# Kernel optimization log

Measured on AMD Instinct MI355X. Metric: run time of the kernel, lower is better.

## Reference

```python
import math
import jax, jax.numpy as jnp
import numpy as np

B, S, D, H = 1, 4096, 1024, 16
HD = D // H


def setup_inputs() -> dict:
    key = jax.random.key(0)
    ks = jax.random.split(key, 11)
    s = 0.02
    inp = {
        "q": jax.random.normal(ks[0], (B, S, D), jnp.float32),
        "k": jax.random.normal(ks[1], (B, S, D), jnp.float32),
        "v": jax.random.normal(ks[2], (B, S, D), jnp.float32),
        # causal boolean mask, broadcastable over [B, H, S, S]
        "mask": jnp.tril(jnp.ones((S, S), jnp.bool_))[None, None],
        "Wq": jax.random.normal(ks[3], (D, D), jnp.float32) * s,
        "bq": jnp.zeros((D,), jnp.float32),
        "Wk": jax.random.normal(ks[4], (D, D), jnp.float32) * s,
        "bk": jnp.zeros((D,), jnp.float32),
        "Wv": jax.random.normal(ks[5], (D, D), jnp.float32) * s,
        "bv": jnp.zeros((D,), jnp.float32),
        "Wo": jax.random.normal(ks[6], (D, D), jnp.float32) * s,
        "bo": jnp.zeros((D,), jnp.float32),
    }
    return inp


def reference(q, k, v, mask, Wq, bq, Wk, bk, Wv, bv, Wo, bo):
    # projections (torch Linear: x @ W.T + b; here W is stored already transposed)
    qp = (q @ Wq + bq).reshape(B, S, H, HD)
    kp = (k @ Wk + bk).reshape(B, S, H, HD)
    vp = (v @ Wv + bv).reshape(B, S, H, HD)
    # scores: [B, H, S, S]
    scores = jnp.einsum("bqhd,bkhd->bhqk", qp, kp) / math.sqrt(HD)
    scores = jnp.where(mask, scores, -jnp.inf)
    attn = jax.nn.softmax(scores, axis=-1)
    # context: [B, H, S, HD] -> [B, S, D]
    ctx = jnp.einsum("bhqk,bkhd->bqhd", attn, vp).reshape(B, S, D)
    return ctx @ Wo + bo
```

## Files before the change

### kernel.cpp

```cpp
#include <hip/hip_runtime.h>
#include <hip/hip_bf16.h>


#define S_LEN 4096
#define D_DIM 1024
#define NHEAD 16
#define HDIM  64

typedef __hip_bfloat16 bf16;
typedef __attribute__((ext_vector_type(8))) short bf16x8v;
typedef __attribute__((ext_vector_type(4))) short bf16x4v;
typedef __attribute__((ext_vector_type(4))) float f32x4;

#define MFMA16(a, b, c) __builtin_amdgcn_mfma_f32_16x16x32_bf16((a), (b), (c), 0, 0, 0)
#define LOG2E 1.44269504088896340736f

__device__ __forceinline__ void async_cp16(const void* g, void* l) {
    __builtin_amdgcn_global_load_lds(
        (const __attribute__((address_space(1))) unsigned int*)g,
        (__attribute__((address_space(3))) unsigned int*)l, 16, 0, 0);
}

__device__ __forceinline__ short bf_bits(float x) {
    union { bf16 h; short s; } u; u.h = __float2bfloat16(x); return u.s;
}

__global__ __launch_bounds__(256) void cvt_bf16_k(
    const float* __restrict__ x0, const float* __restrict__ x1,
    const float* __restrict__ x2,
    bf16* __restrict__ y0, bf16* __restrict__ y1, bf16* __restrict__ y2)
{
    const float* x = (blockIdx.z == 0) ? x0 : (blockIdx.z == 1) ? x1 : x2;
    bf16*       y = (blockIdx.z == 0) ? y0 : (blockIdx.z == 1) ? y1 : y2;
    const size_t i = ((size_t)blockIdx.x * 256 + threadIdx.x);
    const float4 v = ((const float4*)x)[i];
    union { bf16 h[4]; short4 s; } u;
    u.h[0] = __float2bfloat16(v.x);
    u.h[1] = __float2bfloat16(v.y);
    u.h[2] = __float2bfloat16(v.z);
    u.h[3] = __float2bfloat16(v.w);
    ((short4*)y)[i] = u.s;
}

__global__ __launch_bounds__(256) void transpose_cvt_k(
    const float* __restrict__ W0, const float* __restrict__ W1,
    const float* __restrict__ W2, const float* __restrict__ W3,
    bf16* __restrict__ T0, bf16* __restrict__ T1,
    bf16* __restrict__ T2, bf16* __restrict__ T3)
{
    const float* W = (blockIdx.z == 0) ? W0 : (blockIdx.z == 1) ? W1
                   : (blockIdx.z == 2) ? W2 : W3;
    bf16*       Wt = (blockIdx.z == 0) ? T0 : (blockIdx.z == 1) ? T1
                   : (blockIdx.z == 2) ? T2 : T3;
    __shared__ float t[32][33];
    const int bx = blockIdx.x << 5, by = blockIdx.y << 5;
    const int tx = threadIdx.x & 31, ty = threadIdx.x >> 5;
#pragma unroll
    for (int i = 0; i < 32; i += 8)
        t[ty + i][tx] = W[(size_t)(by + ty + i) * D_DIM + bx + tx];
    __syncthreads();
#pragma unroll
    for (int i = 0; i < 32; i += 8)
        Wt[(size_t)(bx + ty + i) * D_DIM + by + tx] = __float2bfloat16(t[tx][ty + i]);
}

struct GemmJob {
    const bf16* A; const bf16* Wt; const float* bias; void* out;
    int mode; float scale;
};

__global__ __launch_bounds__(256) void gemm_k(GemmJob j0, GemmJob j1, GemmJob j2)
{
    const GemmJob j = (blockIdx.z == 0) ? j0 : (blockIdx.z == 1) ? j1 : j2;
    const int K = D_DIM;
    const int bn = blockIdx.x << 7;
    const int bm = blockIdx.y << 7;
    const int tid = threadIdx.x;
    const int w = tid >> 6, lane = tid & 63;
    const int col = lane & 15, g = lane >> 4;
    const int wr = (w >> 1) << 6, wc = (w & 1) << 6;

    __shared__ bf16 As[128 * 64];
    __shared__ bf16 Bs[128 * 64];

    f32x4 acc[4][4];
#pragma unroll
    for (int i = 0; i < 4; ++i)
#pragma unroll
        for (int jj = 0; jj < 4; ++jj) acc[i][jj] = (f32x4){0.f, 0.f, 0.f, 0.f};

    for (int kb = 0; kb < K; kb += 64) {
        __syncthreads();
#pragma unroll
        for (int e = 0; e < 4; ++e) {
            const int lin = (e << 8) + tid;
            const int row = lin >> 3, kcs = lin & 7;
            const int kcg = kcs ^ (row & 7);
            async_cp16(j.A  + (size_t)(bm + row) * K + kb + (kcg << 3), &As[lin << 3]);
            async_cp16(j.Wt + (size_t)(bn + row) * K + kb + (kcg << 3), &Bs[lin << 3]);
        }
        __syncthreads();

#pragma unroll
        for (int s = 0; s < 2; ++s) {
            bf16x8v af[4], bfv[4];
#pragma unroll
            for (int i = 0; i < 4; ++i) {
                const int row = wr + (i << 4) + col;
                af[i] = *(const bf16x8v*)&As[(((row << 3) + (((s << 2) + g) ^ (row & 7)))) << 3];
            }
#pragma unroll
            for (int jj = 0; jj < 4; ++jj) {
                const int row = wc + (jj << 4) + col;
                bfv[jj] = *(const bf16x8v*)&Bs[(((row << 3) + (((s << 2) + g) ^ (row & 7)))) << 3];
            }
#pragma unroll
            for (int i = 0; i < 4; ++i)
#pragma unroll
                for (int jj = 0; jj < 4; ++jj)
                    acc[i][jj] = MFMA16(af[i], bfv[jj], acc[i][jj]);
        }
    }

#pragma unroll
    for (int i = 0; i < 4; ++i)
#pragma unroll
    for (int jj = 0; jj < 4; ++jj)
#pragma unroll
    for (int reg = 0; reg < 4; ++reg) {
        const int row = bm + wr + (i << 4) + (g << 2) + reg;
        const int cg  = bn + wc + (jj << 4) + col;
        const float vv = (acc[i][jj][reg] + j.bias[cg]) * j.scale;
        if (j.mode == 0)
            ((bf16*)j.out)[(((size_t)(cg >> 6)) * S_LEN + row) * HDIM + (cg & 63)] =
                __float2bfloat16(vv);
        else if (j.mode == 2)
            ((bf16*)j.out)[((size_t)(cg >> 6) * HDIM + (cg & 63)) * S_LEN + row] =
                __float2bfloat16(vv);
        else
            ((float*)j.out)[(size_t)row * D_DIM + cg] = vv;
    }
}

__global__ __launch_bounds__(256) void attn_mfma_k(
    const bf16* __restrict__ Qp, const bf16* __restrict__ Kp,
    const bf16* __restrict__ Vt, bf16* __restrict__ ctx)
{
    __shared__ bf16 Ks[2][4096];
    __shared__ bf16 Vs[2][4096];
    __shared__ bf16 Ps[4][1024];

    const int bid = blockIdx.x;
    const int qb  = 63 - (bid >> 4);
    const int h   = bid & 15;
    const int q0  = qb << 6;
    const int tid = threadIdx.x, w = tid >> 6, lane = tid & 63;
    const int col = lane & 15, g = lane >> 4;

    const bf16* Kh = Kp + (size_t)h * S_LEN * HDIM;
    const bf16* Vh = Vt + (size_t)h * HDIM * S_LEN;

    const size_t qrow_base = ((size_t)h * S_LEN + q0 + (w << 4) + col) * HDIM + (g << 3);
    const bf16x8v qf0 = *(const bf16x8v*)(Qp + qrow_base);
    const bf16x8v qf1 = *(const bf16x8v*)(Qp + qrow_base + 32);

    float pl = 0.f;
    f32x4 acco[4];
#pragma unroll
    for (int t = 0; t < 4; ++t) acco[t] = (f32x4){0.f, 0.f, 0.f, 0.f};

    const int nkb = qb + 1;

#pragma unroll
    for (int e = 0; e < 2; ++e) {
        const int lin = (e << 8) + tid;
        const int t = lin >> 7, G = (lin >> 4) & 7, c = lin & 15;
        async_cp16(Kh + (size_t)((t << 4) + c) * HDIM + (G << 3), &Ks[0][lin << 3]);
        async_cp16(Vh + (size_t)((t << 4) + c) * S_LEN + (G << 3), &Vs[0][lin << 3]);
    }

    for (int kb = 0; kb < nkb; ++kb) {
        const int kk0 = kb << 6;
        __syncthreads();
        if (kb + 1 < nkb) {
            const int nk0 = (kb + 1) << 6;
            const int nb  = (kb + 1) & 1;
#pragma unroll
            for (int e = 0; e < 2; ++e) {
                const int lin = (e << 8) + tid;
                const int t = lin >> 7, G = (lin >> 4) & 7, c = lin & 15;
                async_cp16(Kh + (size_t)(nk0 + (t << 4) + c) * HDIM + (G << 3),
                           &Ks[nb][lin << 3]);
                async_cp16(Vh + (size_t)((t << 4) + c) * S_LEN + nk0 + (G << 3),
                           &Vs[nb][lin << 3]);
            }
        }
        const bf16* K0 = Ks[kb & 1];
        const bf16* V0 = Vs[kb & 1];

        f32x4 sa[4];
#pragma unroll
        for (int t = 0; t < 4; ++t) sa[t] = (f32x4){0.f, 0.f, 0.f, 0.f};
#pragma unroll
        for (int t = 0; t < 4; ++t) {
            const bf16x8v kf0 = *(const bf16x8v*)&K0[((t << 7) + (g << 4) + col) << 3];
            const bf16x8v kf1 = *(const bf16x8v*)&K0[((t << 7) + 64 + (g << 4) + col) << 3];
            sa[t] = MFMA16(kf0, qf0, sa[t]);
            sa[t] = MFMA16(kf1, qf1, sa[t]);
        }

        const bool lastt = (kb == nkb - 1);
        const int qq = (w << 4) + col;
#pragma unroll
        for (int t = 0; t < 4; ++t) {
            float p[4];
#pragma unroll
            for (int reg = 0; reg < 4; ++reg) {
                const int krel = (t << 4) + (g << 2) + reg;
                p[reg] = (lastt && krel > qq) ? 0.f
                       : __builtin_amdgcn_exp2f(sa[t][reg]);
            }
            pl += (p[0] + p[1]) + (p[2] + p[3]);
            bf16x4v pv = { bf_bits(p[0]), bf_bits(p[1]), bf_bits(p[2]), bf_bits(p[3]) };
            const int off = (((((t << 1) + (g >> 1)) << 4) + col) << 3) + ((g & 1) << 2);
            *(bf16x4v*)&Ps[w][off] = pv;
        }

        const bf16x8v pf0 = *(const bf16x8v*)&Ps[w][((g << 4) + col) << 3];
        const bf16x8v pf1 = *(const bf16x8v*)&Ps[w][(((4 + g) << 4) + col) << 3];
#pragma unroll
        for (int t = 0; t < 4; ++t) {
            const bf16x8v vf0 = *(const bf16x8v*)&V0[((t << 7) + (g << 4) + col) << 3];
            const bf16x8v vf1 = *(const bf16x8v*)&V0[((t << 7) + 64 + (g << 4) + col) << 3];
            acco[t] = MFMA16(pf0, vf0, acco[t]);
            acco[t] = MFMA16(pf1, vf1, acco[t]);
        }
    }

    float l = pl;
    l += __shfl_xor(l, 16);
    l += __shfl_xor(l, 32);
    float lr[4];
#pragma unroll
    for (int reg = 0; reg < 4; ++reg) lr[reg] = __shfl(l, (g << 2) + reg);

#pragma unroll
    for (int t = 0; t < 4; ++t)
#pragma unroll
        for (int reg = 0; reg < 4; ++reg) {
            const int row = q0 + (w << 4) + (g << 2) + reg;
            ctx[(size_t)row * D_DIM + h * HDIM + (t << 4) + col] =
                __float2bfloat16(acco[t][reg] / lr[reg]);
        }
}

extern "C" void kernel_launch(void* const* d_in, const int* in_sizes, int n_in,
                              void* d_out, int out_size, void* d_ws, size_t ws_size,
                              hipStream_t stream)
{
    const float* q  = (const float*)d_in[0];
    const float* k  = (const float*)d_in[1];
    const float* v  = (const float*)d_in[2];
    const float* Wq = (const float*)d_in[4];
    const float* bq = (const float*)d_in[5];
    const float* Wk = (const float*)d_in[6];
    const float* bk = (const float*)d_in[7];
    const float* Wv = (const float*)d_in[8];
    const float* bv = (const float*)d_in[9];
    const float* Wo = (const float*)d_in[10];
    const float* bo = (const float*)d_in[11];

    const size_t PE  = (size_t)S_LEN * D_DIM;
    const size_t WTE = (size_t)D_DIM * D_DIM;
    const float qscale = 0.125f * LOG2E;

    const dim3 tg(32, 32, 4);
    const dim3 gg(D_DIM / 128, S_LEN / 128, 1);
    const dim3 gg3(D_DIM / 128, S_LEN / 128, 3);
    const dim3 cg((unsigned)(PE / 1024), 1, 3);

    if (ws_size >= (size_t)64 * 1024 * 1024) {
        bf16* Qb = (bf16*)d_ws;
        bf16* Kb = Qb + PE;
        bf16* Vb = Kb + PE;
        bf16* Qp = Vb + PE;
        bf16* Kp = Qp + PE;
        bf16* Vt = Kp + PE;
        bf16* Wtq = Vt + PE;
        bf16* Wtk = Wtq + WTE;
        bf16* Wtv = Wtk + WTE;
        bf16* Wto = Wtv + WTE;
        bf16* ctx = Qb;

        transpose_cvt_k<<<tg, 256, 0, stream>>>(Wq, Wk, Wv, Wo, Wtq, Wtk, Wtv, Wto);
        cvt_bf16_k<<<cg, 256, 0, stream>>>(q, k, v, Qb, Kb, Vb);

        GemmJob jq{Qb, Wtq, bq, Qp, 0, qscale};
        GemmJob jk{Kb, Wtk, bk, Kp, 0, 1.0f};
        GemmJob jv{Vb, Wtv, bv, Vt, 2, 1.0f};
        gemm_k<<<gg3, 256, 0, stream>>>(jq, jk, jv);

        attn_mfma_k<<<dim3(1024), 256, 0, stream>>>(Qp, Kp, Vt, ctx);

        GemmJob jo{ctx, Wto, bo, d_out, 1, 1.0f};
        gemm_k<<<gg, 256, 0, stream>>>(jo, jo, jo);
    } else {
        bf16* X  = (bf16*)d_ws;
        bf16* Qp = X + PE;
        bf16* Kp = Qp + PE;
        bf16* Vt = Kp + PE;
        bf16* Wtq = Vt + PE;
        bf16* Wtk = Wtq + WTE;
        bf16* Wtv = Wtk + WTE;
        bf16* Wto = Wtv + WTE;

        transpose_cvt_k<<<tg, 256, 0, stream>>>(Wq, Wk, Wv, Wo, Wtq, Wtk, Wtv, Wto);

        const dim3 cg1((unsigned)(PE / 1024), 1, 1);
        cvt_bf16_k<<<cg1, 256, 0, stream>>>(q, q, q, X, X, X);
        GemmJob jq{X, Wtq, bq, Qp, 0, qscale};
        gemm_k<<<gg, 256, 0, stream>>>(jq, jq, jq);
        cvt_bf16_k<<<cg1, 256, 0, stream>>>(k, k, k, X, X, X);
        GemmJob jk{X, Wtk, bk, Kp, 0, 1.0f};
        gemm_k<<<gg, 256, 0, stream>>>(jk, jk, jk);
        cvt_bf16_k<<<cg1, 256, 0, stream>>>(v, v, v, X, X, X);
        GemmJob jv{X, Wtv, bv, Vt, 2, 1.0f};
        gemm_k<<<gg, 256, 0, stream>>>(jv, jv, jv);

        attn_mfma_k<<<dim3(1024), 256, 0, stream>>>(Qp, Kp, Vt, X);

        GemmJob jo{X, Wto, bo, d_out, 1, 1.0f};
        gemm_k<<<gg, 256, 0, stream>>>(jo, jo, jo);
    }
}
```

Measured before the change: 344.4 us.

## Pair causal query blocks per attention workgroup and shrink GEMM N-tile

The attention kernel now gives each workgroup two query blocks (pr and 63-pr) for one head. They share the K/V tile loads, which balances the causal triangle's work across workgroups and halves the grid to 512. The P scratch in LDS gets an XOR swizzle to reduce bank conflicts. The GEMM tile narrows from 128x128 to 128x64 to launch more workgroups for the projection GEMMs, at the cost of less operand reuse per tile and more registers and branching in attention.

```diff
diff --git a/kernel.cpp b/kernel.cpp
--- a/kernel.cpp
+++ b/kernel.cpp
@@ -73,21 +73,21 @@
 {
     const GemmJob j = (blockIdx.z == 0) ? j0 : (blockIdx.z == 1) ? j1 : j2;
     const int K = D_DIM;
-    const int bn = blockIdx.x << 7;
+    const int bn = blockIdx.x << 6;
     const int bm = blockIdx.y << 7;
     const int tid = threadIdx.x;
     const int w = tid >> 6, lane = tid & 63;
     const int col = lane & 15, g = lane >> 4;
-    const int wr = (w >> 1) << 6, wc = (w & 1) << 6;
+    const int wr = (w >> 1) << 6, wc = (w & 1) << 5;
 
     __shared__ bf16 As[128 * 64];
-    __shared__ bf16 Bs[128 * 64];
-
-    f32x4 acc[4][4];
+    __shared__ bf16 Bs[64 * 64];
+
+    f32x4 acc[4][2];
 #pragma unroll
     for (int i = 0; i < 4; ++i)
 #pragma unroll
-        for (int jj = 0; jj < 4; ++jj) acc[i][jj] = (f32x4){0.f, 0.f, 0.f, 0.f};
+        for (int jj = 0; jj < 2; ++jj) acc[i][jj] = (f32x4){0.f, 0.f, 0.f, 0.f};
 
     for (int kb = 0; kb < K; kb += 64) {
         __syncthreads();
@@ -96,28 +96,34 @@
             const int lin = (e << 8) + tid;
             const int row = lin >> 3, kcs = lin & 7;
             const int kcg = kcs ^ (row & 7);
-            async_cp16(j.A  + (size_t)(bm + row) * K + kb + (kcg << 3), &As[lin << 3]);
+            async_cp16(j.A + (size_t)(bm + row) * K + kb + (kcg << 3), &As[lin << 3]);
+        }
+#pragma unroll
+        for (int e = 0; e < 2; ++e) {
+            const int lin = (e << 8) + tid;
+            const int row = lin >> 3, kcs = lin & 7;
+            const int kcg = kcs ^ (row & 7);
             async_cp16(j.Wt + (size_t)(bn + row) * K + kb + (kcg << 3), &Bs[lin << 3]);
         }
         __syncthreads();
 
 #pragma unroll
         for (int s = 0; s < 2; ++s) {
-            bf16x8v af[4], bfv[4];
+            bf16x8v af[4], bfv[2];
 #pragma unroll
             for (int i = 0; i < 4; ++i) {
                 const int row = wr + (i << 4) + col;
-                af[i] = *(const bf16x8v*)&As[(((row << 3) + (((s << 2) + g) ^ (row & 7)))) << 3];
-            }
-#pragma unroll
-            for (int jj = 0; jj < 4; ++jj) {
+                af[i] = *(const bf16x8v*)&As[((row << 3) + (((s << 2) + g) ^ (row & 7))) << 3];
+            }
+#pragma unroll
+            for (int jj = 0; jj < 2; ++jj) {
                 const int row = wc + (jj << 4) + col;
-                bfv[jj] = *(const bf16x8v*)&Bs[(((row << 3) + (((s << 2) + g) ^ (row & 7)))) << 3];
+                bfv[jj] = *(const bf16x8v*)&Bs[((row << 3) + (((s << 2) + g) ^ (row & 7))) << 3];
             }
 #pragma unroll
             for (int i = 0; i < 4; ++i)
 #pragma unroll
-                for (int jj = 0; jj < 4; ++jj)
+                for (int jj = 0; jj < 2; ++jj)
                     acc[i][jj] = MFMA16(af[i], bfv[jj], acc[i][jj]);
         }
     }
@@ -125,7 +131,7 @@
 #pragma unroll
     for (int i = 0; i < 4; ++i)
 #pragma unroll
-    for (int jj = 0; jj < 4; ++jj)
+    for (int jj = 0; jj < 2; ++jj)
 #pragma unroll
     for (int reg = 0; reg < 4; ++reg) {
         const int row = bm + wr + (i << 4) + (g << 2) + reg;
@@ -148,28 +154,45 @@
 {
     __shared__ bf16 Ks[2][4096];
     __shared__ bf16 Vs[2][4096];
-    __shared__ bf16 Ps[4][1024];
+    __shared__ bf16 PsA[4][1024];
+    __shared__ bf16 PsB[4][1024];
 
     const int bid = blockIdx.x;
-    const int qb  = 63 - (bid >> 4);
+    const int pr  = bid >> 4;
     const int h   = bid & 15;
-    const int q0  = qb << 6;
+    const int qbA = pr, qbB = 63 - pr;
+    const int qA0 = qbA << 6, qB0 = qbB << 6;
+    const int nkbA = qbA + 1, nkbB = qbB + 1;
     const int tid = threadIdx.x, w = tid >> 6, lane = tid & 63;
     const int col = lane & 15, g = lane >> 4;
 
     const bf16* Kh = Kp + (size_t)h * S_LEN * HDIM;
     const bf16* Vh = Vt + (size_t)h * HDIM * S_LEN;
 
-    const size_t qrow_base = ((size_t)h * S_LEN + q0 + (w << 4) + col) * HDIM + (g << 3);
-    const bf16x8v qf0 = *(const bf16x8v*)(Qp + qrow_base);
-    const bf16x8v qf1 = *(const bf16x8v*)(Qp + qrow_base + 32);
-
-    float pl = 0.f;
-    f32x4 acco[4];
-#pragma unroll
-    for (int t = 0; t < 4; ++t) acco[t] = (f32x4){0.f, 0.f, 0.f, 0.f};
-
-    const int nkb = qb + 1;
+    const size_t qbaseA = ((size_t)h * S_LEN + qA0 + (w << 4) + col) * HDIM + (g << 3);
+    const bf16x8v qfA0 = *(const bf16x8v*)(Qp + qbaseA);
+    const bf16x8v qfA1 = *(const bf16x8v*)(Qp + qbaseA + 32);
+    const size_t qbaseB = ((size_t)h * S_LEN + qB0 + (w << 4) + col) * HDIM + (g << 3);
+    const bf16x8v qfB0 = *(const bf16x8v*)(Qp + qbaseB);
+    const bf16x8v qfB1 = *(const bf16x8v*)(Qp + qbaseB + 32);
+
+    int pwoff[4];
+#pragma unroll
+    for (int t = 0; t < 4; ++t) {
+        const int Gk = (t << 1) + (g >> 1);
+        pwoff[t] = (((Gk << 4) + (col ^ ((Gk & 3) << 2))) << 3) + ((g & 1) << 2);
+    }
+    const int proff0 = (((g) << 4) + (col ^ ((g & 3) << 2))) << 3;
+    const int proff1 = (((4 + g) << 4) + (col ^ ((g & 3) << 2))) << 3;
+
+    float plA = 0.f, plB = 0.f;
+    f32x4 accoA[4], accoB[4];
+#pragma unroll
+    for (int t = 0; t < 4; ++t) {
+        accoA[t] = (f32x4){0.f, 0.f, 0.f, 0.f};
+        accoB[t] = (f32x4){0.f, 0.f, 0.f, 0.f};
+    }
+    const int qq = (w << 4) + col;
 
 #pragma unroll
     for (int e = 0; e < 2; ++e) {
@@ -179,10 +202,9 @@
         async_cp16(Vh + (size_t)((t << 4) + c) * S_LEN + (G << 3), &Vs[0][lin << 3]);
     }
 
-    for (int kb = 0; kb < nkb; ++kb) {
-        const int kk0 = kb << 6;
+    for (int kb = 0; kb < nkbB; ++kb) {
         __syncthreads();
-        if (kb + 1 < nkb) {
+        if (kb + 1 < nkbB) {
             const int nk0 = (kb + 1) << 6;
             const int nb  = (kb + 1) & 1;
 #pragma unroll
@@ -197,61 +219,94 @@
         }
         const bf16* K0 = Ks[kb & 1];
         const bf16* V0 = Vs[kb & 1];
-
-        f32x4 sa[4];
-#pragma unroll
-        for (int t = 0; t < 4; ++t) sa[t] = (f32x4){0.f, 0.f, 0.f, 0.f};
+        const bool doA = (kb < nkbA);
+
+        f32x4 saA[4], saB[4];
+#pragma unroll
+        for (int t = 0; t < 4; ++t) {
+            saA[t] = (f32x4){0.f, 0.f, 0.f, 0.f};
+            saB[t] = (f32x4){0.f, 0.f, 0.f, 0.f};
+        }
 #pragma unroll
         for (int t = 0; t < 4; ++t) {
             const bf16x8v kf0 = *(const bf16x8v*)&K0[((t << 7) + (g << 4) + col) << 3];
             const bf16x8v kf1 = *(const bf16x8v*)&K0[((t << 7) + 64 + (g << 4) + col) << 3];
-            sa[t] = MFMA16(kf0, qf0, sa[t]);
-            sa[t] = MFMA16(kf1, qf1, sa[t]);
-        }
-
-        const bool lastt = (kb == nkb - 1);
-        const int qq = (w << 4) + col;
+            saB[t] = MFMA16(kf0, qfB0, saB[t]);
+            saB[t] = MFMA16(kf1, qfB1, saB[t]);
+            if (doA) {
+                saA[t] = MFMA16(kf0, qfA0, saA[t]);
+                saA[t] = MFMA16(kf1, qfA1, saA[t]);
+            }
+        }
+
+        const bool lastB = (kb == nkbB - 1);
 #pragma unroll
         for (int t = 0; t < 4; ++t) {
             float p[4];
 #pragma unroll
             for (int reg = 0; reg < 4; ++reg) {
                 const int krel = (t << 4) + (g << 2) + reg;
-                p[reg] = (lastt && krel > qq) ? 0.f
-                       : __builtin_amdgcn_exp2f(sa[t][reg]);
-            }
-            pl += (p[0] + p[1]) + (p[2] + p[3]);
+                p[reg] = (lastB && krel > qq) ? 0.f
+                       : __builtin_amdgcn_exp2f(saB[t][reg]);
+            }
+            plB += (p[0] + p[1]) + (p[2] + p[3]);
             bf16x4v pv = { bf_bits(p[0]), bf_bits(p[1]), bf_bits(p[2]), bf_bits(p[3]) };
-            const int off = (((((t << 1) + (g >> 1)) << 4) + col) << 3) + ((g & 1) << 2);
-            *(bf16x4v*)&Ps[w][off] = pv;
-        }
-
-        const bf16x8v pf0 = *(const bf16x8v*)&Ps[w][((g << 4) + col) << 3];
-        const bf16x8v pf1 = *(const bf16x8v*)&Ps[w][(((4 + g) << 4) + col) << 3];
+            *(bf16x4v*)&PsB[w][pwoff[t]] = pv;
+        }
+        if (doA) {
+            const bool lastA = (kb == nkbA - 1);
+#pragma unroll
+            for (int t = 0; t < 4; ++t) {
+                float p[4];
+#pragma unroll
+                for (int reg = 0; reg < 4; ++reg) {
+                    const int krel = (t << 4) + (g << 2) + reg;
+                    p[reg] = (lastA && krel > qq) ? 0.f
+                           : __builtin_amdgcn_exp2f(saA[t][reg]);
+                }
+                plA += (p[0] + p[1]) + (p[2] + p[3]);
+                bf16x4v pv = { bf_bits(p[0]), bf_bits(p[1]), bf_bits(p[2]), bf_bits(p[3]) };
+                *(bf16x4v*)&PsA[w][pwoff[t]] = pv;
+            }
+        }
+
+        const bf16x8v pfB0 = *(const bf16x8v*)&PsB[w][proff0];
+        const bf16x8v pfB1 = *(const bf16x8v*)&PsB[w][proff1];
+        bf16x8v pfA0, pfA1;
+        if (doA) {
+            pfA0 = *(const bf16x8v*)&PsA[w][proff0];
+            pfA1 = *(const bf16x8v*)&PsA[w][proff1];
+        }
 #pragma unroll
         for (int t = 0; t < 4; ++t) {
             const bf16x8v vf0 = *(const bf16x8v*)&V0[((t << 7) + (g << 4) + col) << 3];
             const bf16x8v vf1 = *(const bf16x8v*)&V0[((t << 7) + 64 + (g << 4) + col) << 3];
-            acco[t] = MFMA16(pf0, vf0, acco[t]);
-            acco[t] = MFMA16(pf1, vf1, acco[t]);
-        }
-    }
-
-    float l = pl;
-    l += __shfl_xor(l, 16);
-    l += __shfl_xor(l, 32);
-    float lr[4];
-#pragma unroll
-    for (int reg = 0; reg < 4; ++reg) lr[reg] = __shfl(l, (g << 2) + reg);
-
-#pragma unroll
-    for (int t = 0; t < 4; ++t)
-#pragma unroll
-        for (int reg = 0; reg < 4; ++reg) {
-            const int row = q0 + (w << 4) + (g << 2) + reg;
-            ctx[(size_t)row * D_DIM + h * HDIM + (t << 4) + col] =
-                __float2bfloat16(acco[t][reg] / lr[reg]);
-        }
+            accoB[t] = MFMA16(pfB0, vf0, accoB[t]);
+            accoB[t] = MFMA16(pfB1, vf1, accoB[t]);
+            if (doA) {
+                accoA[t] = MFMA16(pfA0, vf0, accoA[t]);
+                accoA[t] = MFMA16(pfA1, vf1, accoA[t]);
+            }
+        }
+    }
+
+    float lA = plA, lB = plB;
+    lA += __shfl_xor(lA, 16); lA += __shfl_xor(lA, 32);
+    lB += __shfl_xor(lB, 16); lB += __shfl_xor(lB, 32);
+#pragma unroll
+    for (int reg = 0; reg < 4; ++reg) {
+        const float lrA = __shfl(lA, (g << 2) + reg);
+        const float lrB = __shfl(lB, (g << 2) + reg);
+#pragma unroll
+        for (int t = 0; t < 4; ++t) {
+            const int rowA = qA0 + (w << 4) + (g << 2) + reg;
+            const int rowB = qB0 + (w << 4) + (g << 2) + reg;
+            ctx[(size_t)rowA * D_DIM + h * HDIM + (t << 4) + col] =
+                __float2bfloat16(accoA[t][reg] / lrA);
+            ctx[(size_t)rowB * D_DIM + h * HDIM + (t << 4) + col] =
+                __float2bfloat16(accoB[t][reg] / lrB);
+        }
+    }
 }
 
 extern "C" void kernel_launch(void* const* d_in, const int* in_sizes, int n_in,
@@ -275,8 +330,8 @@
     const float qscale = 0.125f * LOG2E;
 
     const dim3 tg(32, 32, 4);
-    const dim3 gg(D_DIM / 128, S_LEN / 128, 1);
-    const dim3 gg3(D_DIM / 128, S_LEN / 128, 3);
+    const dim3 gg(D_DIM / 64, S_LEN / 128, 1);
+    const dim3 gg3(D_DIM / 64, S_LEN / 128, 3);
     const dim3 cg((unsigned)(PE / 1024), 1, 3);
 
     if (ws_size >= (size_t)64 * 1024 * 1024) {
@@ -300,7 +355,7 @@
         GemmJob jv{Vb, Wtv, bv, Vt, 2, 1.0f};
         gemm_k<<<gg3, 256, 0, stream>>>(jq, jk, jv);
 
-        attn_mfma_k<<<dim3(1024), 256, 0, stream>>>(Qp, Kp, Vt, ctx);
+        attn_mfma_k<<<dim3(512), 256, 0, stream>>>(Qp, Kp, Vt, ctx);
 
         GemmJob jo{ctx, Wto, bo, d_out, 1, 1.0f};
         gemm_k<<<gg, 256, 0, stream>>>(jo, jo, jo);
@@ -327,7 +382,7 @@
         GemmJob jv{X, Wtv, bv, Vt, 2, 1.0f};
         gemm_k<<<gg, 256, 0, stream>>>(jv, jv, jv);
 
-        attn_mfma_k<<<dim3(1024), 256, 0, stream>>>(Qp, Kp, Vt, X);
+        attn_mfma_k<<<dim3(512), 256, 0, stream>>>(Qp, Kp, Vt, X);
 
         GemmJob jo{X, Wto, bo, d_out, 1, 1.0f};
         gemm_k<<<gg, 256, 0, stream>>>(jo, jo, jo);
```

After: 337.9 us. Within noise of the previous version (-1.9%).
